# Kernel optimization log

Hardware: AMD Instinct MI355X
Metric: run time of the kernel (lower is better)

Reference implementation:

```python
import jax, jax.numpy as jnp
import numpy as np

N = 100000
E = 1600000
IN_DIM, HID_DIM, OUT_DIM = 128, 64, 32
HEADS = 8
NEG_SLOPE = 0.2
NEG_INF = -1e9


def _glorot(key, shape):
    stdv = np.sqrt(6.0 / (shape[-2] + shape[-1]))
    return jax.random.uniform(key, shape, jnp.float32, -stdv, stdv)


def gat_conv(x, src, dst, self_mask, W, att, bias, heads, out_ch, concat):
    """One GATConv layer (eval mode: dropout off). src/dst already include self-loops;
    self_mask marks original edges that were self-loops (removed via -inf score)."""
    n = x.shape[0]
    h = (x @ W).reshape(n, heads, out_ch)              # [N,H,C]
    x_i = h[dst]                                        # [Etot,H,C] gather target
    x_j = h[src]                                        # [Etot,H,C] gather source
    a = jnp.einsum('ehc,hc->eh', x_i, att[0, :, :out_ch]) \
        + jnp.einsum('ehc,hc->eh', x_j, att[0, :, out_ch:])
    alpha = jax.nn.leaky_relu(a, NEG_SLOPE)             # [Etot,H]
    alpha = jnp.where(self_mask[:, None], NEG_INF, alpha)
    amax = jax.lax.stop_gradient(
        jax.ops.segment_max(alpha, dst, num_segments=n))
    ex = jnp.exp(alpha - amax[dst])
    denom = jax.ops.segment_sum(ex, dst, num_segments=n)
    w = ex / denom[dst]                                 # segment softmax over incoming edges
    out = jax.ops.segment_sum(x_j * w[:, :, None], dst, num_segments=n)  # [N,H,C]
    out = out.reshape(n, heads * out_ch) if concat else out.mean(axis=1)
    return out + bias


def setup_inputs() -> dict:
    key = jax.random.key(0)
    ks = jax.random.split(key, 12)
    x = jax.random.normal(ks[0], (N, IN_DIM), jnp.float32)
    edge_index = jax.random.randint(ks[1], (2, E), 0, N, jnp.int64)
    c1 = HID_DIM // HEADS  # 8
    params = {
        'W1': _glorot(ks[2], (IN_DIM, HEADS * c1)),
        'att1': _glorot(ks[3], (1, HEADS, 2 * c1)),
        'b1': jnp.zeros((HID_DIM,), jnp.float32),
        'W2': _glorot(ks[4], (HID_DIM, HEADS * c1)),
        'att2': _glorot(ks[5], (1, HEADS, 2 * c1)),
        'b2': jnp.zeros((HID_DIM,), jnp.float32),
        'W3': _glorot(ks[6], (HID_DIM, 1 * OUT_DIM)),
        'att3': _glorot(ks[7], (1, 1, 2 * OUT_DIM)),
        'b3': jnp.zeros((OUT_DIM,), jnp.float32),
    }
    return dict(x=x, edge_index=edge_index, **params)


def reference(x, edge_index, W1, att1, b1, W2, att2, b2, W3, att3, b3):
    n = x.shape[0]
    src, dst = edge_index[0], edge_index[1]
    loop = jnp.arange(n, dtype=src.dtype)
    src_f = jnp.concatenate([src, loop])
    dst_f = jnp.concatenate([dst, loop])
    # remove_self_loops + add_self_loops: mask original self-loops, append fresh ones
    self_mask = jnp.concatenate([src == dst, jnp.zeros((n,), bool)])
    c1 = HID_DIM // HEADS
    h = jax.nn.elu(gat_conv(x, src_f, dst_f, self_mask, W1, att1, b1, HEADS, c1, True))
    h = jax.nn.elu(gat_conv(h, src_f, dst_f, self_mask, W2, att2, b2, HEADS, c1, True))
    out = gat_conv(h, src_f, dst_f, self_mask, W3, att3, b3, 1, OUT_DIM, False)
    return out
```

## Files before the change

kernel.cpp:

```cpp
#include <hip/hip_runtime.h>
#include <hip/hip_bf16.h>

#define NN 100000
#define EE 1600000

constexpr int SCAN_BLK = 1024;
constexpr int NB_SCAN  = (NN + SCAN_BLK - 1) / SCAN_BLK;

constexpr int NR2 = 8;
constexpr int RSZ = NN / NR2;
constexpr int CH  = 32;
constexpr int CSZ = EE / CH;


__global__ __launch_bounds__(256) void histL_k(const int* __restrict__ ei,
                                               int* __restrict__ CntG) {
    __shared__ int cnt[RSZ];
    int r = blockIdx.x % NR2, c = blockIdx.x / NR2;
    int lo = r * RSZ;
    for (int t = threadIdx.x; t < RSZ; t += 256) cnt[t] = 0;
    __syncthreads();
    const int* __restrict__ dstp = ei + EE;
    int base = c * CSZ;
    int tid = threadIdx.x;
    for (int ii = 0; ii < CSZ; ii += 1024) {
        int d[4], s[4];
        #pragma unroll
        for (int k = 0; k < 4; ++k) {
            int off = ii + tid + k * 256;
            bool v = off < CSZ;
            d[k] = v ? dstp[base + off] : -1;
            s[k] = v ? ei[base + off]   : -1;
        }
        #pragma unroll
        for (int k = 0; k < 4; ++k) {
            int dl = d[k] - lo;
            if (dl >= 0 && dl < RSZ && s[k] != d[k]) atomicAdd(&cnt[dl], 1);
        }
    }
    __syncthreads();
    for (int t = threadIdx.x; t < RSZ; t += 256)
        CntG[(size_t)c * NN + lo + t] = cnt[t];
}

__global__ void combineL_k(int* __restrict__ CntG, int* __restrict__ deg) {
    int d = blockIdx.x * 256 + threadIdx.x;
    if (d < NN) {
        int run = 0;
        #pragma unroll 8
        for (int c = 0; c < CH; ++c) {
            int v = CntG[(size_t)c * NN + d];
            CntG[(size_t)c * NN + d] = run;
            run += v;
        }
        deg[d] = run;
    }
}

__global__ void sum_blocks(const int* __restrict__ deg, int* __restrict__ partials) {
    __shared__ int sh[256];
    int t = threadIdx.x;
    int base = blockIdx.x * SCAN_BLK + t * 4;
    int s = 0;
    #pragma unroll
    for (int k = 0; k < 4; ++k) { int i = base + k; if (i < NN) s += deg[i]; }
    sh[t] = s; __syncthreads();
    for (int off = 128; off > 0; off >>= 1) {
        if (t < off) sh[t] += sh[t + off];
        __syncthreads();
    }
    if (t == 0) partials[blockIdx.x] = sh[0];
}

__global__ void scan_partials(int* __restrict__ partials) {
    __shared__ int sh[128];
    int t = threadIdx.x;
    int v = (t < NB_SCAN) ? partials[t] : 0;
    sh[t] = v;
    __syncthreads();
    for (int off = 1; off < 128; off <<= 1) {
        int tmp = (t >= off) ? sh[t - off] : 0;
        __syncthreads();
        sh[t] += tmp;
        __syncthreads();
    }
    if (t < NB_SCAN) partials[t] = sh[t] - v;
}

__global__ void scan_final(const int* __restrict__ deg, const int* __restrict__ partials,
                           int* __restrict__ rowptr) {
    __shared__ int sh[256];
    int t = threadIdx.x;
    int base = blockIdx.x * SCAN_BLK + t * 4;
    int v[4]; int s = 0;
    #pragma unroll
    for (int k = 0; k < 4; ++k) { int i = base + k; v[k] = (i < NN) ? deg[i] : 0; s += v[k]; }
    sh[t] = s; __syncthreads();
    for (int off = 1; off < 256; off <<= 1) {
        int tmp = (t >= off) ? sh[t - off] : 0;
        __syncthreads();
        sh[t] += tmp;
        __syncthreads();
    }
    int pref = partials[blockIdx.x] + sh[t] - s;
    #pragma unroll
    for (int k = 0; k < 4; ++k) {
        int i = base + k;
        if (i < NN) {
            rowptr[i] = pref; pref += v[k];
            if (i == NN - 1) rowptr[NN] = pref;
        }
    }
}

__global__ __launch_bounds__(256) void scatterL_k(const int* __restrict__ ei,
                                                  const int* __restrict__ CntG,
                                                  const int* __restrict__ rowptr,
                                                  int* __restrict__ col) {
    __shared__ int cur[RSZ];
    int r = blockIdx.x % NR2, c = blockIdx.x / NR2;
    int lo = r * RSZ;
    for (int t = threadIdx.x; t < RSZ; t += 256)
        cur[t] = rowptr[lo + t] + CntG[(size_t)c * NN + lo + t];
    __syncthreads();
    const int* __restrict__ dstp = ei + EE;
    int base = c * CSZ;
    int tid = threadIdx.x;
    for (int ii = 0; ii < CSZ; ii += 1024) {
        int d[4], s[4];
        #pragma unroll
        for (int k = 0; k < 4; ++k) {
            int off = ii + tid + k * 256;
            bool v = off < CSZ;
            d[k] = v ? dstp[base + off] : -1;
            s[k] = v ? ei[base + off]   : -1;
        }
        #pragma unroll
        for (int k = 0; k < 4; ++k) {
            int dl = d[k] - lo;
            if (dl >= 0 && dl < RSZ && s[k] != d[k]) {
                int p = atomicAdd(&cur[dl], 1);
                col[p] = s[k];
            }
        }
    }
}


template<int K, int M, int H, int NPB>
__global__ __launch_bounds__(256) void gemm_tile(const float* __restrict__ xin,
                          const float* __restrict__ W,
                          const float* __restrict__ att,
                          uint2* __restrict__ Hbf,
                          float* __restrict__ ssrcA,
                          float* __restrict__ sdst) {
    constexpr int C   = M / H;
    constexpr int MG  = M / 4;
    constexpr int NG  = NPB / 4;
    static_assert(MG * NG == 256, "tile mismatch");
    constexpr int K4  = K / 4;
    constexpr int KC4 = (K4 > 16) ? 16 : K4;
    constexpr int NCH = K4 / KC4;

    __shared__ float4 Wq[K * MG];
    __shared__ float4 Xq[NPB * KC4];

    int tid = threadIdx.x;
    const float4* W4 = (const float4*)W;
    for (int i = tid; i < K * MG; i += 256) Wq[i] = W4[i];

    int node0 = blockIdx.x * NPB;
    const float4* x4 = (const float4*)xin;

    int mg = tid % MG, ng = tid / MG;
    int nb = ng * 4;
    float acc[4][4];
    #pragma unroll
    for (int i = 0; i < 4; ++i)
        #pragma unroll
        for (int j = 0; j < 4; ++j) acc[i][j] = 0.f;

    for (int ch = 0; ch < NCH; ++ch) {
        __syncthreads();
        for (int i = tid; i < NPB * KC4; i += 256) {
            int n = i / KC4, k4l = i % KC4;
            int node = node0 + n;
            float4 v = make_float4(0.f, 0.f, 0.f, 0.f);
            if (node < NN) v = x4[(size_t)node * K4 + ch * KC4 + k4l];
            Xq[i] = v;
        }
        __syncthreads();
        #pragma unroll 4
        for (int k4 = 0; k4 < KC4; ++k4) {
            float4 xv[4], wv[4];
            #pragma unroll
            for (int i = 0; i < 4; ++i) xv[i] = Xq[(nb + i) * KC4 + k4];
            int kbase = (ch * KC4 + k4) * 4;
            #pragma unroll
            for (int kk = 0; kk < 4; ++kk) wv[kk] = Wq[(kbase + kk) * MG + mg];
            #pragma unroll
            for (int i = 0; i < 4; ++i) {
                const float* xf = (const float*)&xv[i];
                #pragma unroll
                for (int kk = 0; kk < 4; ++kk) {
                    const float* wf = (const float*)&wv[kk];
                    float xs = xf[kk];
                    acc[i][0] = fmaf(xs, wf[0], acc[i][0]);
                    acc[i][1] = fmaf(xs, wf[1], acc[i][1]);
                    acc[i][2] = fmaf(xs, wf[2], acc[i][2]);
                    acc[i][3] = fmaf(xs, wf[3], acc[i][3]);
                }
            }
        }
    }

    constexpr int TPH = C / 4;
    int head = mg / TPH;
    int c0   = (mg % TPH) * 4;
    float ad[4], as_[4];
    #pragma unroll
    for (int j = 0; j < 4; ++j) {
        ad[j]  = att[head * 2 * C + c0 + j];
        as_[j] = att[head * 2 * C + C + c0 + j];
    }
    #pragma unroll
    for (int i = 0; i < 4; ++i) {
        int node = node0 + nb + i;
        if (node < NN) {
            unsigned short us[4];
            #pragma unroll
            for (int j = 0; j < 4; ++j) {
                __hip_bfloat16 b = __float2bfloat16(acc[i][j]);
                us[j] = *(unsigned short*)&b;
            }
            uint2 pk;
            pk.x = (unsigned)us[0] | ((unsigned)us[1] << 16);
            pk.y = (unsigned)us[2] | ((unsigned)us[3] << 16);
            Hbf[(size_t)node * MG + mg] = pk;
        }
        float pd = acc[i][0]*ad[0]  + acc[i][1]*ad[1]  + acc[i][2]*ad[2]  + acc[i][3]*ad[3];
        float ps = acc[i][0]*as_[0] + acc[i][1]*as_[1] + acc[i][2]*as_[2] + acc[i][3]*as_[3];
        #pragma unroll
        for (int off = 1; off < TPH; off <<= 1) {
            pd += __shfl_xor(pd, off, 64);
            ps += __shfl_xor(ps, off, 64);
        }
        if ((mg % TPH) == 0 && node < NN) {
            sdst[node * H + head]  = pd;
            ssrcA[node * H + head] = ps;
        }
    }
}


template<int CT, int H, int U, bool ELU_OUT>
__global__ __launch_bounds__(256) void agg_k(const int* __restrict__ rowptr, const int* __restrict__ col,
                      const float* __restrict__ sdst, const float* __restrict__ ssrcA,
                      const uint2* __restrict__ Hbf,
                      const float* __restrict__ bias, float* __restrict__ output) {
    constexpr int C    = CT / H;
    constexpr int CP   = CT / 4;
    constexpr int G    = 64 / CP;
    constexpr int NL   = U / G;
    constexpr int EPEL = (U * H >= 64) ? (U * H) / 64 : 1;
    static_assert(EPEL == 1 || EPEL == 2, "mapping");

    int lane = threadIdx.x & 63;
    int node = blockIdx.x * (blockDim.x >> 6) + (threadIdx.x >> 6);
    if (node >= NN) return;

    int cp = lane % CP;
    int pp = lane / CP;
    int hh = (4 * cp) / C;
    int eh = lane % H;
    int gb = lane / H;

    float sd = (lane < U * H) ? sdst[node * H + eh] : 0.f;

    int start = rowptr[node], end = rowptr[node + 1];
    int total = end + 1;
    float4 acc = make_float4(0.f, 0.f, 0.f, 0.f);
    float dsum = 0.f;

    for (int j = start; j < total; j += U) {
        int cv = node;
        {
            int idx = j + lane;
            if (lane < U && idx < end) cv = col[idx];
        }
        float e1 = 0.f, e2 = 0.f;
        if (EPEL == 2) {
            int b1 = __shfl(cv, gb, 64);
            int b2 = __shfl(cv, gb + U / 2, 64);
            float s1 = ssrcA[b1 * H + eh];
            float s2 = ssrcA[b2 * H + eh];
            float a1 = sd + s1; a1 = (a1 >= 0.f) ? a1 : 0.2f * a1;
            float a2 = sd + s2; a2 = (a2 >= 0.f) ? a2 : 0.2f * a2;
            if (j + gb < total)          e1 = __expf(a1);
            if (j + gb + U / 2 < total)  e2 = __expf(a2);
            dsum += e1 + e2;
        } else {
            if (lane < U * H) {
                int b1 = __shfl(cv, gb, 64);
                float s1 = ssrcA[b1 * H + eh];
                float a1 = sd + s1; a1 = (a1 >= 0.f) ? a1 : 0.2f * a1;
                if (j + gb < total) e1 = __expf(a1);
                dsum += e1;
            }
        }
        uint2 hv[NL];
        #pragma unroll
        for (int t = 0; t < NL; ++t) {
            int se = __shfl(cv, t * G + pp, 64);
            hv[t] = Hbf[(size_t)se * CP + cp];
        }
        #pragma unroll
        for (int t = 0; t < NL; ++t) {
            int eidx = t * G + pp;
            float ex;
            if (EPEL == 2)
                ex = __shfl((t * G + G - 1 < U / 2) ? e1 : e2, (eidx & (U / 2 - 1)) * H + hh, 64);
            else
                ex = __shfl(e1, eidx * H + hh, 64);
            float f0 = __uint_as_float(hv[t].x << 16);
            float f1 = __uint_as_float(hv[t].x & 0xffff0000u);
            float f2 = __uint_as_float(hv[t].y << 16);
            float f3 = __uint_as_float(hv[t].y & 0xffff0000u);
            acc.x = fmaf(ex, f0, acc.x);
            acc.y = fmaf(ex, f1, acc.y);
            acc.z = fmaf(ex, f2, acc.z);
            acc.w = fmaf(ex, f3, acc.w);
        }
    }
    #pragma unroll
    for (int off = H; off < 64; off <<= 1) dsum += __shfl_xor(dsum, off, 64);
    float den = __shfl(dsum, hh, 64);
    #pragma unroll
    for (int off = CP; off < 64; off <<= 1) {
        acc.x += __shfl_xor(acc.x, off, 64);
        acc.y += __shfl_xor(acc.y, off, 64);
        acc.z += __shfl_xor(acc.z, off, 64);
        acc.w += __shfl_xor(acc.w, off, 64);
    }
    if (lane < CP) {
        float inv = 1.f / den;
        float4 bv = ((const float4*)bias)[cp];
        float4 v;
        v.x = acc.x * inv + bv.x;
        v.y = acc.y * inv + bv.y;
        v.z = acc.z * inv + bv.z;
        v.w = acc.w * inv + bv.w;
        if (ELU_OUT) {
            v.x = (v.x > 0.f) ? v.x : expm1f(v.x);
            v.y = (v.y > 0.f) ? v.y : expm1f(v.y);
            v.z = (v.z > 0.f) ? v.z : expm1f(v.z);
            v.w = (v.w > 0.f) ? v.w : expm1f(v.w);
        }
        ((float4*)output)[(size_t)node * CP + cp] = v;
    }
}


extern "C" void kernel_launch(void* const* d_in, const int* in_sizes, int n_in,
                              void* d_out, int out_size, void* d_ws, size_t ws_size,
                              hipStream_t stream) {
    const float* x    = (const float*)d_in[0];
    const int*   ei   = (const int*)d_in[1];
    const float* W1   = (const float*)d_in[2];
    const float* att1 = (const float*)d_in[3];
    const float* b1   = (const float*)d_in[4];
    const float* W2   = (const float*)d_in[5];
    const float* att2 = (const float*)d_in[6];
    const float* b2   = (const float*)d_in[7];
    const float* W3   = (const float*)d_in[8];
    const float* att3 = (const float*)d_in[9];
    const float* b3   = (const float*)d_in[10];
    float* out = (float*)d_out;

    char* p = (char*)d_ws;
    auto alloc = [&](size_t bytes) -> void* {
        void* r = (void*)p;
        p += (bytes + 255) & ~(size_t)255;
        return r;
    };
    int*   rowptr   = (int*)alloc((NN + 1) * sizeof(int));
    int*   deg      = (int*)alloc(NN * sizeof(int));
    int*   CntG     = (int*)alloc((size_t)CH * NN * sizeof(int));
    int*   partials = (int*)alloc(NB_SCAN * sizeof(int));
    int*   col      = (int*)alloc(EE * sizeof(int));
    float* sdst     = (float*)alloc((size_t)NN * 8 * sizeof(float));
    float* ssrcA    = (float*)alloc((size_t)NN * 8 * sizeof(float));
    uint2* Hbf      = (uint2*)alloc((size_t)NN * 16 * sizeof(uint2));
    float* Fb       = (float*)alloc((size_t)NN * 64 * sizeof(float));

    histL_k<<<CH * NR2, 256, 0, stream>>>(ei, CntG);
    combineL_k<<<(NN + 255) / 256, 256, 0, stream>>>(CntG, deg);
    sum_blocks<<<NB_SCAN, 256, 0, stream>>>(deg, partials);
    scan_partials<<<1, 128, 0, stream>>>(partials);
    scan_final<<<NB_SCAN, 256, 0, stream>>>(deg, partials, rowptr);
    scatterL_k<<<CH * NR2, 256, 0, stream>>>(ei, CntG, rowptr, col);

    gemm_tile<128, 64, 8, 64><<<(NN + 63) / 64, 256, 0, stream>>>(x, W1, att1, Hbf, ssrcA, sdst);
    agg_k<64, 8, 16, true><<<(NN + 3) / 4, 256, 0, stream>>>(rowptr, col, sdst, ssrcA, Hbf, b1, Fb);

    gemm_tile<64, 64, 8, 64><<<(NN + 63) / 64, 256, 0, stream>>>(Fb, W2, att2, Hbf, ssrcA, sdst);
    agg_k<64, 8, 16, true><<<(NN + 3) / 4, 256, 0, stream>>>(rowptr, col, sdst, ssrcA, Hbf, b2, Fb);

    gemm_tile<64, 32, 1, 128><<<(NN + 127) / 128, 256, 0, stream>>>(Fb, W3, att3, Hbf, ssrcA, sdst);
    agg_k<32, 1, 32, false><<<(NN + 3) / 4, 256, 0, stream>>>(rowptr, col, sdst, ssrcA, Hbf, b3, out);
}
```

Measured before the change: 424.5 us.

## Process two destination nodes per wavefront in GAT aggregation to overlap gathers

Each wavefront now handles two adjacent destination nodes and interleaves their edge loops, so the gathers of source features and attention scores for both nodes are in flight together. The self-loop contribution is hoisted out of the edge loop and computed once per node up front, rather than being folded into the loop as an extra edge. This aims to hide gather latency in the memory-bound aggregation through more independent loads per wave. In exchange it raises register pressure, halves the wave count, and can leave lanes idle when the two nodes have different degrees.

```diff
diff --git a/kernel.cpp b/kernel.cpp
--- a/kernel.cpp
+++ b/kernel.cpp
@@ -266,97 +266,225 @@
     static_assert(EPEL == 1 || EPEL == 2, "mapping");
 
     int lane = threadIdx.x & 63;
-    int node = blockIdx.x * (blockDim.x >> 6) + (threadIdx.x >> 6);
-    if (node >= NN) return;
+    int wid  = threadIdx.x >> 6;
+    int nA = blockIdx.x * ((blockDim.x >> 6) * 2) + wid * 2;
+    if (nA >= NN) return;
+    int nB = nA + 1;
+    bool hasB = (nB < NN);
 
     int cp = lane % CP;
     int pp = lane / CP;
     int hh = (4 * cp) / C;
     int eh = lane % H;
     int gb = lane / H;
-
-    float sd = (lane < U * H) ? sdst[node * H + eh] : 0.f;
-
-    int start = rowptr[node], end = rowptr[node + 1];
-    int total = end + 1;
-    float4 acc = make_float4(0.f, 0.f, 0.f, 0.f);
-    float dsum = 0.f;
-
-    for (int j = start; j < total; j += U) {
-        int cv = node;
-        {
-            int idx = j + lane;
-            if (lane < U && idx < end) cv = col[idx];
-        }
-        float e1 = 0.f, e2 = 0.f;
+    bool elane = (lane < U * H);
+
+    float sdA = elane ? sdst[nA * H + eh] : 0.f;
+    float sdB = (hasB && elane) ? sdst[nB * H + eh] : 0.f;
+
+    int startA = rowptr[nA], endA = rowptr[nA + 1];
+    int startB = 0, endB = 0;
+    if (hasB) { startB = endA; endB = rowptr[nB + 1]; }
+
+    float dsumA = 0.f, dsumB = 0.f;
+    float esA = 0.f, esB = 0.f;
+    if (lane < H) {
+        float ss = ssrcA[nA * H + lane];
+        float a = sdA + ss; a = (a >= 0.f) ? a : 0.2f * a;
+        esA = __expf(a);
+        dsumA = esA;
+    }
+    if (hasB && lane < H) {
+        float ss = ssrcA[nB * H + lane];
+        float a = sdB + ss; a = (a >= 0.f) ? a : 0.2f * a;
+        esB = __expf(a);
+        dsumB = esB;
+    }
+    uint2 hsA = Hbf[(size_t)nA * CP + cp];
+    uint2 hsB = make_uint2(0u, 0u);
+    if (hasB) hsB = Hbf[(size_t)nB * CP + cp];
+    float exsA = __shfl(esA, hh, 64);
+    float exsB = __shfl(esB, hh, 64);
+    float4 accA = make_float4(0.f, 0.f, 0.f, 0.f);
+    float4 accB = make_float4(0.f, 0.f, 0.f, 0.f);
+    if (pp == 0) {
+        accA.x = exsA * __uint_as_float(hsA.x << 16);
+        accA.y = exsA * __uint_as_float(hsA.x & 0xffff0000u);
+        accA.z = exsA * __uint_as_float(hsA.y << 16);
+        accA.w = exsA * __uint_as_float(hsA.y & 0xffff0000u);
+        accB.x = exsB * __uint_as_float(hsB.x << 16);
+        accB.y = exsB * __uint_as_float(hsB.x & 0xffff0000u);
+        accB.z = exsB * __uint_as_float(hsB.y << 16);
+        accB.w = exsB * __uint_as_float(hsB.y & 0xffff0000u);
+    }
+
+    int jA = startA, jB = startB;
+    while (jA < endA || jB < endB) {
+        bool doA = jA < endA;
+        bool doB = jB < endB;
+
+        int cvA = nA, cvB = nB;
+        if (doA) { int idx = jA + lane; if (lane < U && idx < endA) cvA = col[idx]; }
+        if (doB) { int idx = jB + lane; if (lane < U && idx < endB) cvB = col[idx]; }
+
+        float s1A = 0.f, s2A = 0.f, s1B = 0.f, s2B = 0.f;
         if (EPEL == 2) {
-            int b1 = __shfl(cv, gb, 64);
-            int b2 = __shfl(cv, gb + U / 2, 64);
-            float s1 = ssrcA[b1 * H + eh];
-            float s2 = ssrcA[b2 * H + eh];
-            float a1 = sd + s1; a1 = (a1 >= 0.f) ? a1 : 0.2f * a1;
-            float a2 = sd + s2; a2 = (a2 >= 0.f) ? a2 : 0.2f * a2;
-            if (j + gb < total)          e1 = __expf(a1);
-            if (j + gb + U / 2 < total)  e2 = __expf(a2);
-            dsum += e1 + e2;
+            int b1A = __shfl(cvA, gb, 64), b2A = __shfl(cvA, gb + U / 2, 64);
+            int b1B = __shfl(cvB, gb, 64), b2B = __shfl(cvB, gb + U / 2, 64);
+            if (doA) {
+                if (jA + gb < endA)         s1A = ssrcA[b1A * H + eh];
+                if (jA + gb + U / 2 < endA) s2A = ssrcA[b2A * H + eh];
+            }
+            if (doB) {
+                if (jB + gb < endB)         s1B = ssrcA[b1B * H + eh];
+                if (jB + gb + U / 2 < endB) s2B = ssrcA[b2B * H + eh];
+            }
         } else {
-            if (lane < U * H) {
-                int b1 = __shfl(cv, gb, 64);
-                float s1 = ssrcA[b1 * H + eh];
-                float a1 = sd + s1; a1 = (a1 >= 0.f) ? a1 : 0.2f * a1;
-                if (j + gb < total) e1 = __expf(a1);
-                dsum += e1;
-            }
-        }
-        uint2 hv[NL];
-        #pragma unroll
-        for (int t = 0; t < NL; ++t) {
-            int se = __shfl(cv, t * G + pp, 64);
-            hv[t] = Hbf[(size_t)se * CP + cp];
-        }
-        #pragma unroll
-        for (int t = 0; t < NL; ++t) {
-            int eidx = t * G + pp;
-            float ex;
-            if (EPEL == 2)
-                ex = __shfl((t * G + G - 1 < U / 2) ? e1 : e2, (eidx & (U / 2 - 1)) * H + hh, 64);
-            else
-                ex = __shfl(e1, eidx * H + hh, 64);
-            float f0 = __uint_as_float(hv[t].x << 16);
-            float f1 = __uint_as_float(hv[t].x & 0xffff0000u);
-            float f2 = __uint_as_float(hv[t].y << 16);
-            float f3 = __uint_as_float(hv[t].y & 0xffff0000u);
-            acc.x = fmaf(ex, f0, acc.x);
-            acc.y = fmaf(ex, f1, acc.y);
-            acc.z = fmaf(ex, f2, acc.z);
-            acc.w = fmaf(ex, f3, acc.w);
-        }
-    }
-    #pragma unroll
-    for (int off = H; off < 64; off <<= 1) dsum += __shfl_xor(dsum, off, 64);
-    float den = __shfl(dsum, hh, 64);
+            int b1A = __shfl(cvA, gb, 64);
+            int b1B = __shfl(cvB, gb, 64);
+            if (doA && elane && jA + gb < endA) s1A = ssrcA[b1A * H + eh];
+            if (doB && elane && jB + gb < endB) s1B = ssrcA[b1B * H + eh];
+        }
+
+        uint2 hvA[NL], hvB[NL];
+        if (doA) {
+            #pragma unroll
+            for (int t = 0; t < NL; ++t) {
+                int se = __shfl(cvA, t * G + pp, 64);
+                hvA[t] = Hbf[(size_t)se * CP + cp];
+            }
+        }
+        if (doB) {
+            #pragma unroll
+            for (int t = 0; t < NL; ++t) {
+                int se = __shfl(cvB, t * G + pp, 64);
+                hvB[t] = Hbf[(size_t)se * CP + cp];
+            }
+        }
+
+        float e1A = 0.f, e2A = 0.f, e1B = 0.f, e2B = 0.f;
+        if (EPEL == 2) {
+            if (doA) {
+                float a1 = sdA + s1A; a1 = (a1 >= 0.f) ? a1 : 0.2f * a1;
+                float a2 = sdA + s2A; a2 = (a2 >= 0.f) ? a2 : 0.2f * a2;
+                if (jA + gb < endA)         e1A = __expf(a1);
+                if (jA + gb + U / 2 < endA) e2A = __expf(a2);
+                dsumA += e1A + e2A;
+            }
+            if (doB) {
+                float a1 = sdB + s1B; a1 = (a1 >= 0.f) ? a1 : 0.2f * a1;
+                float a2 = sdB + s2B; a2 = (a2 >= 0.f) ? a2 : 0.2f * a2;
+                if (jB + gb < endB)         e1B = __expf(a1);
+                if (jB + gb + U / 2 < endB) e2B = __expf(a2);
+                dsumB += e1B + e2B;
+            }
+        } else {
+            if (doA) {
+                float a1 = sdA + s1A; a1 = (a1 >= 0.f) ? a1 : 0.2f * a1;
+                if (elane && jA + gb < endA) { e1A = __expf(a1); dsumA += e1A; }
+            }
+            if (doB) {
+                float a1 = sdB + s1B; a1 = (a1 >= 0.f) ? a1 : 0.2f * a1;
+                if (elane && jB + gb < endB) { e1B = __expf(a1); dsumB += e1B; }
+            }
+        }
+
+        if (doA) {
+            #pragma unroll
+            for (int t = 0; t < NL; ++t) {
+                int eidx = t * G + pp;
+                float ex;
+                if (EPEL == 2)
+                    ex = __shfl((t * G + G - 1 < U / 2) ? e1A : e2A, (eidx & (U / 2 - 1)) * H + hh, 64);
+                else
+                    ex = __shfl(e1A, eidx * H + hh, 64);
+                float f0 = __uint_as_float(hvA[t].x << 16);
+                float f1 = __uint_as_float(hvA[t].x & 0xffff0000u);
+                float f2 = __uint_as_float(hvA[t].y << 16);
+                float f3 = __uint_as_float(hvA[t].y & 0xffff0000u);
+                accA.x = fmaf(ex, f0, accA.x);
+                accA.y = fmaf(ex, f1, accA.y);
+                accA.z = fmaf(ex, f2, accA.z);
+                accA.w = fmaf(ex, f3, accA.w);
+            }
+            jA += U;
+        }
+        if (doB) {
+            #pragma unroll
+            for (int t = 0; t < NL; ++t) {
+                int eidx = t * G + pp;
+                float ex;
+                if (EPEL == 2)
+                    ex = __shfl((t * G + G - 1 < U / 2) ? e1B : e2B, (eidx & (U / 2 - 1)) * H + hh, 64);
+                else
+                    ex = __shfl(e1B, eidx * H + hh, 64);
+                float f0 = __uint_as_float(hvB[t].x << 16);
+                float f1 = __uint_as_float(hvB[t].x & 0xffff0000u);
+                float f2 = __uint_as_float(hvB[t].y << 16);
+                float f3 = __uint_as_float(hvB[t].y & 0xffff0000u);
+                accB.x = fmaf(ex, f0, accB.x);
+                accB.y = fmaf(ex, f1, accB.y);
+                accB.z = fmaf(ex, f2, accB.z);
+                accB.w = fmaf(ex, f3, accB.w);
+            }
+            jB += U;
+        }
+    }
+
+    #pragma unroll
+    for (int off = H; off < 64; off <<= 1) dsumA += __shfl_xor(dsumA, off, 64);
+    float denA = __shfl(dsumA, hh, 64);
     #pragma unroll
     for (int off = CP; off < 64; off <<= 1) {
-        acc.x += __shfl_xor(acc.x, off, 64);
-        acc.y += __shfl_xor(acc.y, off, 64);
-        acc.z += __shfl_xor(acc.z, off, 64);
-        acc.w += __shfl_xor(acc.w, off, 64);
+        accA.x += __shfl_xor(accA.x, off, 64);
+        accA.y += __shfl_xor(accA.y, off, 64);
+        accA.z += __shfl_xor(accA.z, off, 64);
+        accA.w += __shfl_xor(accA.w, off, 64);
     }
     if (lane < CP) {
-        float inv = 1.f / den;
+        float inv = 1.f / denA;
         float4 bv = ((const float4*)bias)[cp];
         float4 v;
-        v.x = acc.x * inv + bv.x;
-        v.y = acc.y * inv + bv.y;
-        v.z = acc.z * inv + bv.z;
-        v.w = acc.w * inv + bv.w;
+        v.x = accA.x * inv + bv.x;
+        v.y = accA.y * inv + bv.y;
+        v.z = accA.z * inv + bv.z;
+        v.w = accA.w * inv + bv.w;
         if (ELU_OUT) {
             v.x = (v.x > 0.f) ? v.x : expm1f(v.x);
             v.y = (v.y > 0.f) ? v.y : expm1f(v.y);
             v.z = (v.z > 0.f) ? v.z : expm1f(v.z);
             v.w = (v.w > 0.f) ? v.w : expm1f(v.w);
         }
-        ((float4*)output)[(size_t)node * CP + cp] = v;
+        ((float4*)output)[(size_t)nA * CP + cp] = v;
+    }
+
+    if (hasB) {
+        #pragma unroll
+        for (int off = H; off < 64; off <<= 1) dsumB += __shfl_xor(dsumB, off, 64);
+        float denB = __shfl(dsumB, hh, 64);
+        #pragma unroll
+        for (int off = CP; off < 64; off <<= 1) {
+            accB.x += __shfl_xor(accB.x, off, 64);
+            accB.y += __shfl_xor(accB.y, off, 64);
+            accB.z += __shfl_xor(accB.z, off, 64);
+            accB.w += __shfl_xor(accB.w, off, 64);
+        }
+        if (lane < CP) {
+            float inv = 1.f / denB;
+            float4 bv = ((const float4*)bias)[cp];
+            float4 v;
+            v.x = accB.x * inv + bv.x;
+            v.y = accB.y * inv + bv.y;
+            v.z = accB.z * inv + bv.z;
+            v.w = accB.w * inv + bv.w;
+            if (ELU_OUT) {
+                v.x = (v.x > 0.f) ? v.x : expm1f(v.x);
+                v.y = (v.y > 0.f) ? v.y : expm1f(v.y);
+                v.z = (v.z > 0.f) ? v.z : expm1f(v.z);
+                v.w = (v.w > 0.f) ? v.w : expm1f(v.w);
+            }
+            ((float4*)output)[(size_t)nB * CP + cp] = v;
+        }
     }
 }
 
@@ -401,11 +529,11 @@
     scatterL_k<<<CH * NR2, 256, 0, stream>>>(ei, CntG, rowptr, col);
 
     gemm_tile<128, 64, 8, 64><<<(NN + 63) / 64, 256, 0, stream>>>(x, W1, att1, Hbf, ssrcA, sdst);
-    agg_k<64, 8, 16, true><<<(NN + 3) / 4, 256, 0, stream>>>(rowptr, col, sdst, ssrcA, Hbf, b1, Fb);
+    agg_k<64, 8, 16, true><<<(NN + 7) / 8, 256, 0, stream>>>(rowptr, col, sdst, ssrcA, Hbf, b1, Fb);
 
     gemm_tile<64, 64, 8, 64><<<(NN + 63) / 64, 256, 0, stream>>>(Fb, W2, att2, Hbf, ssrcA, sdst);
-    agg_k<64, 8, 16, true><<<(NN + 3) / 4, 256, 0, stream>>>(rowptr, col, sdst, ssrcA, Hbf, b2, Fb);
+    agg_k<64, 8, 16, true><<<(NN + 7) / 8, 256, 0, stream>>>(rowptr, col, sdst, ssrcA, Hbf, b2, Fb);
 
     gemm_tile<64, 32, 1, 128><<<(NN + 127) / 128, 256, 0, stream>>>(Fb, W3, att3, Hbf, ssrcA, sdst);
-    agg_k<32, 1, 32, false><<<(NN + 3) / 4, 256, 0, stream>>>(rowptr, col, sdst, ssrcA, Hbf, b3, out);
-}
+    agg_k<32, 1, 32, false><<<(NN + 7) / 8, 256, 0, stream>>>(rowptr, col, sdst, ssrcA, Hbf, b3, out);
+}
```

Result: slower. 453.6 us (+6.9%).

## Widen aggregation gathers to 16-byte loads, peel self-loop, process 32 edges per step

Applied to the files above, without the earlier changes.

The aggregation kernel now has each lane load 8 bf16 features (uint4) instead of 4, which halves the lanes per node row and doubles the edges covered per shuffle round. The self-loop contribution is computed once before the edge loop, so the loop runs only over real neighbors. Layers 1 and 2 process 32 edges per iteration instead of 16. The aim is fewer, wider gather instructions and more memory-level parallelism per wave, at the cost of more registers (8 accumulators) and possibly more wasted lanes on low-degree nodes.

```diff
diff --git a/kernel.cpp b/kernel.cpp
--- a/kernel.cpp
+++ b/kernel.cpp
@@ -259,11 +259,14 @@
                       const uint2* __restrict__ Hbf,
                       const float* __restrict__ bias, float* __restrict__ output) {
     constexpr int C    = CT / H;
-    constexpr int CP   = CT / 4;
+    constexpr int CP   = CT / 8;
     constexpr int G    = 64 / CP;
     constexpr int NL   = U / G;
     constexpr int EPEL = (U * H >= 64) ? (U * H) / 64 : 1;
-    static_assert(EPEL == 1 || EPEL == 2, "mapping");
+    constexpr int STRIDE = U / EPEL;
+    static_assert(EPEL == 1 || (STRIDE == G && NL == EPEL), "mapping");
+
+    const uint4* __restrict__ Hb4 = (const uint4*)Hbf;
 
     int lane = threadIdx.x & 63;
     int node = blockIdx.x * (blockDim.x >> 6) + (threadIdx.x >> 6);
@@ -271,92 +274,119 @@
 
     int cp = lane % CP;
     int pp = lane / CP;
-    int hh = (4 * cp) / C;
+    int hh = (8 * cp) / C;
     int eh = lane % H;
     int gb = lane / H;
-
-    float sd = (lane < U * H) ? sdst[node * H + eh] : 0.f;
+    bool elane = (lane < U * H);
+
+    float sd = elane ? sdst[node * H + eh] : 0.f;
 
     int start = rowptr[node], end = rowptr[node + 1];
-    int total = end + 1;
-    float4 acc = make_float4(0.f, 0.f, 0.f, 0.f);
+
     float dsum = 0.f;
-
-    for (int j = start; j < total; j += U) {
+    float e_self = 0.f;
+    if (lane < H) {
+        float ss = ssrcA[node * H + lane];
+        float a = sd + ss; a = (a >= 0.f) ? a : 0.2f * a;
+        e_self = __expf(a);
+        dsum = e_self;
+    }
+    uint4 hs = Hb4[(size_t)node * CP + cp];
+    float exs = __shfl(e_self, hh, 64);
+    float acc[8];
+    #pragma unroll
+    for (int q = 0; q < 8; ++q) acc[q] = 0.f;
+    if (pp == 0) {
+        acc[0] = exs * __uint_as_float(hs.x << 16);
+        acc[1] = exs * __uint_as_float(hs.x & 0xffff0000u);
+        acc[2] = exs * __uint_as_float(hs.y << 16);
+        acc[3] = exs * __uint_as_float(hs.y & 0xffff0000u);
+        acc[4] = exs * __uint_as_float(hs.z << 16);
+        acc[5] = exs * __uint_as_float(hs.z & 0xffff0000u);
+        acc[6] = exs * __uint_as_float(hs.w << 16);
+        acc[7] = exs * __uint_as_float(hs.w & 0xffff0000u);
+    }
+
+    for (int j = start; j < end; j += U) {
         int cv = node;
-        {
-            int idx = j + lane;
-            if (lane < U && idx < end) cv = col[idx];
-        }
-        float e1 = 0.f, e2 = 0.f;
-        if (EPEL == 2) {
-            int b1 = __shfl(cv, gb, 64);
-            int b2 = __shfl(cv, gb + U / 2, 64);
-            float s1 = ssrcA[b1 * H + eh];
-            float s2 = ssrcA[b2 * H + eh];
-            float a1 = sd + s1; a1 = (a1 >= 0.f) ? a1 : 0.2f * a1;
-            float a2 = sd + s2; a2 = (a2 >= 0.f) ? a2 : 0.2f * a2;
-            if (j + gb < total)          e1 = __expf(a1);
-            if (j + gb + U / 2 < total)  e2 = __expf(a2);
-            dsum += e1 + e2;
-        } else {
-            if (lane < U * H) {
-                int b1 = __shfl(cv, gb, 64);
-                float s1 = ssrcA[b1 * H + eh];
-                float a1 = sd + s1; a1 = (a1 >= 0.f) ? a1 : 0.2f * a1;
-                if (j + gb < total) e1 = __expf(a1);
-                dsum += e1;
-            }
-        }
-        uint2 hv[NL];
+        { int idx = j + lane; if (lane < U && idx < end) cv = col[idx]; }
+
+        int   b_[EPEL];
+        float sv[EPEL];
+        #pragma unroll
+        for (int k = 0; k < EPEL; ++k) b_[k] = __shfl(cv, gb + k * STRIDE, 64);
+        #pragma unroll
+        for (int k = 0; k < EPEL; ++k) sv[k] = ssrcA[b_[k] * H + eh];
+
+        uint4 hv[NL];
         #pragma unroll
         for (int t = 0; t < NL; ++t) {
             int se = __shfl(cv, t * G + pp, 64);
-            hv[t] = Hbf[(size_t)se * CP + cp];
-        }
+            hv[t] = Hb4[(size_t)se * CP + cp];
+        }
+
+        float e[EPEL];
+        #pragma unroll
+        for (int k = 0; k < EPEL; ++k) {
+            float a = sd + sv[k]; a = (a >= 0.f) ? a : 0.2f * a;
+            float ev = 0.f;
+            bool ok = (EPEL == 1) ? (elane && j + gb < end)
+                                  : (j + gb + k * STRIDE < end);
+            if (ok) ev = __expf(a);
+            e[k] = ev;
+            dsum += ev;
+        }
+
         #pragma unroll
         for (int t = 0; t < NL; ++t) {
-            int eidx = t * G + pp;
             float ex;
-            if (EPEL == 2)
-                ex = __shfl((t * G + G - 1 < U / 2) ? e1 : e2, (eidx & (U / 2 - 1)) * H + hh, 64);
-            else
-                ex = __shfl(e1, eidx * H + hh, 64);
-            float f0 = __uint_as_float(hv[t].x << 16);
-            float f1 = __uint_as_float(hv[t].x & 0xffff0000u);
-            float f2 = __uint_as_float(hv[t].y << 16);
-            float f3 = __uint_as_float(hv[t].y & 0xffff0000u);
-            acc.x = fmaf(ex, f0, acc.x);
-            acc.y = fmaf(ex, f1, acc.y);
-            acc.z = fmaf(ex, f2, acc.z);
-            acc.w = fmaf(ex, f3, acc.w);
-        }
-    }
+            if (EPEL >= 2) ex = __shfl(e[t], pp * H + hh, 64);
+            else           ex = __shfl(e[0], (t * G + pp) * H + hh, 64);
+            acc[0] = fmaf(ex, __uint_as_float(hv[t].x << 16),        acc[0]);
+            acc[1] = fmaf(ex, __uint_as_float(hv[t].x & 0xffff0000u), acc[1]);
+            acc[2] = fmaf(ex, __uint_as_float(hv[t].y << 16),        acc[2]);
+            acc[3] = fmaf(ex, __uint_as_float(hv[t].y & 0xffff0000u), acc[3]);
+            acc[4] = fmaf(ex, __uint_as_float(hv[t].z << 16),        acc[4]);
+            acc[5] = fmaf(ex, __uint_as_float(hv[t].z & 0xffff0000u), acc[5]);
+            acc[6] = fmaf(ex, __uint_as_float(hv[t].w << 16),        acc[6]);
+            acc[7] = fmaf(ex, __uint_as_float(hv[t].w & 0xffff0000u), acc[7]);
+        }
+    }
+
     #pragma unroll
     for (int off = H; off < 64; off <<= 1) dsum += __shfl_xor(dsum, off, 64);
     float den = __shfl(dsum, hh, 64);
     #pragma unroll
     for (int off = CP; off < 64; off <<= 1) {
-        acc.x += __shfl_xor(acc.x, off, 64);
-        acc.y += __shfl_xor(acc.y, off, 64);
-        acc.z += __shfl_xor(acc.z, off, 64);
-        acc.w += __shfl_xor(acc.w, off, 64);
+        #pragma unroll
+        for (int q = 0; q < 8; ++q) acc[q] += __shfl_xor(acc[q], off, 64);
     }
     if (lane < CP) {
         float inv = 1.f / den;
-        float4 bv = ((const float4*)bias)[cp];
-        float4 v;
-        v.x = acc.x * inv + bv.x;
-        v.y = acc.y * inv + bv.y;
-        v.z = acc.z * inv + bv.z;
-        v.w = acc.w * inv + bv.w;
+        const float4* b4 = (const float4*)bias;
+        float4 bv0 = b4[2 * cp], bv1 = b4[2 * cp + 1];
+        float4 v0, v1;
+        v0.x = acc[0] * inv + bv0.x;
+        v0.y = acc[1] * inv + bv0.y;
+        v0.z = acc[2] * inv + bv0.z;
+        v0.w = acc[3] * inv + bv0.w;
+        v1.x = acc[4] * inv + bv1.x;
+        v1.y = acc[5] * inv + bv1.y;
+        v1.z = acc[6] * inv + bv1.z;
+        v1.w = acc[7] * inv + bv1.w;
         if (ELU_OUT) {
-            v.x = (v.x > 0.f) ? v.x : expm1f(v.x);
-            v.y = (v.y > 0.f) ? v.y : expm1f(v.y);
-            v.z = (v.z > 0.f) ? v.z : expm1f(v.z);
-            v.w = (v.w > 0.f) ? v.w : expm1f(v.w);
-        }
-        ((float4*)output)[(size_t)node * CP + cp] = v;
+            v0.x = (v0.x > 0.f) ? v0.x : expm1f(v0.x);
+            v0.y = (v0.y > 0.f) ? v0.y : expm1f(v0.y);
+            v0.z = (v0.z > 0.f) ? v0.z : expm1f(v0.z);
+            v0.w = (v0.w > 0.f) ? v0.w : expm1f(v0.w);
+            v1.x = (v1.x > 0.f) ? v1.x : expm1f(v1.x);
+            v1.y = (v1.y > 0.f) ? v1.y : expm1f(v1.y);
+            v1.z = (v1.z > 0.f) ? v1.z : expm1f(v1.z);
+            v1.w = (v1.w > 0.f) ? v1.w : expm1f(v1.w);
+        }
+        float4* o4 = (float4*)output;
+        o4[(size_t)node * (2 * CP) + 2 * cp]     = v0;
+        o4[(size_t)node * (2 * CP) + 2 * cp + 1] = v1;
     }
 }
 
@@ -401,10 +431,10 @@
     scatterL_k<<<CH * NR2, 256, 0, stream>>>(ei, CntG, rowptr, col);
 
     gemm_tile<128, 64, 8, 64><<<(NN + 63) / 64, 256, 0, stream>>>(x, W1, att1, Hbf, ssrcA, sdst);
-    agg_k<64, 8, 16, true><<<(NN + 3) / 4, 256, 0, stream>>>(rowptr, col, sdst, ssrcA, Hbf, b1, Fb);
+    agg_k<64, 8, 32, true><<<(NN + 3) / 4, 256, 0, stream>>>(rowptr, col, sdst, ssrcA, Hbf, b1, Fb);
 
     gemm_tile<64, 64, 8, 64><<<(NN + 63) / 64, 256, 0, stream>>>(Fb, W2, att2, Hbf, ssrcA, sdst);
-    agg_k<64, 8, 16, true><<<(NN + 3) / 4, 256, 0, stream>>>(rowptr, col, sdst, ssrcA, Hbf, b2, Fb);
+    agg_k<64, 8, 32, true><<<(NN + 3) / 4, 256, 0, stream>>>(rowptr, col, sdst, ssrcA, Hbf, b2, Fb);
 
     gemm_tile<64, 32, 1, 128><<<(NN + 127) / 128, 256, 0, stream>>>(Fb, W3, att3, Hbf, ssrcA, sdst);
     agg_k<32, 1, 32, false><<<(NN + 3) / 4, 256, 0, stream>>>(rowptr, col, sdst, ssrcA, Hbf, b3, out);
```

New measurement: 449.2 us. 5.8% more time.
